# Kernel optimization log

Measured on AMD Instinct MI355X. Metric: run time of the kernel, lower is better.

The kernel has to match this reference:

```python
import jax, jax.numpy as jnp
import numpy as np

NUM_LEVELS = 16
LEVEL_DIM = 2
BASE_RES = 16
MAX_RES = 2048
HASHMAP_SIZE = 1 << 19
N_POINTS = 2000000

# Instant-NGP geometric progression of grid resolutions
_scale = np.exp2(np.log2(MAX_RES / BASE_RES) / (NUM_LEVELS - 1))
RESOLUTIONS = [int(np.ceil(BASE_RES * _scale ** l)) for l in range(NUM_LEVELS)]

# corner offsets of the unit cube, shape [8, 3]
_OFFS = np.stack(np.meshgrid([0, 1], [0, 1], [0, 1], indexing='ij'), -1).reshape(8, 3)
_PRIMES = np.array([1, 2654435761, 805459861], dtype=np.uint32)


def grid_encode(x, table):
    """x: [N,3] in [0,1]; table: [L, T, F] -> [N, L*F]."""
    offs = jnp.asarray(_OFFS, dtype=jnp.int32)          # [8,3]
    feats = []
    for l, res in enumerate(RESOLUTIONS):
        pos = x * (res - 1)                              # [N,3]
        pos_i = jnp.clip(jnp.floor(pos).astype(jnp.int32), 0, res - 2)
        frac = pos - pos_i.astype(pos.dtype)             # [N,3]
        corners = pos_i[:, None, :] + offs[None]         # [N,8,3]
        if res ** 3 <= HASHMAP_SIZE:
            # dense (collision-free) indexing for coarse levels
            idx = corners[..., 0] + res * (corners[..., 1] + res * corners[..., 2])
        else:
            # spatial hash: xor of coordinate * prime, mod table size
            c = corners.astype(jnp.uint32)
            h = (c[..., 0] * _PRIMES[0]) ^ (c[..., 1] * _PRIMES[1]) ^ (c[..., 2] * _PRIMES[2])
            idx = (h % jnp.uint32(HASHMAP_SIZE)).astype(jnp.int32)
        vals = table[l][idx]                             # [N,8,F] gather
        # multilinear interpolation weights per corner
        w = jnp.prod(jnp.where(offs[None].astype(bool), frac[:, None, :], 1.0 - frac[:, None, :]), axis=-1)  # [N,8]
        feats.append(jnp.einsum('nc,ncf->nf', w, vals))
    return jnp.concatenate(feats, axis=-1)               # [N, 32]


def setup_inputs() -> dict:
    key = jax.random.key(0)
    ks = jax.random.split(key, 6)
    x = jax.random.uniform(ks[0], (N_POINTS, 3), dtype=jnp.float32)
    table = jax.random.uniform(ks[1], (NUM_LEVELS, HASHMAP_SIZE, LEVEL_DIM),
                               dtype=jnp.float32, minval=-1e-4, maxval=1e-4)
    in_dim = NUM_LEVELS * LEVEL_DIM  # 32
    W1 = jax.random.normal(ks[2], (in_dim, 64), dtype=jnp.float32) / np.sqrt(in_dim)
    W2 = jax.random.normal(ks[3], (64, 64), dtype=jnp.float32) / 8.0
    W3 = jax.random.normal(ks[4], (64, 64), dtype=jnp.float32) / 8.0
    Wo = jax.random.normal(ks[5], (64, 1), dtype=jnp.float32) / 8.0
    z = lambda n: jnp.zeros((n,), dtype=jnp.float32)
    return {"x": x, "table": table, "W1": W1, "b1": z(64), "W2": W2, "b2": z(64),
            "W3": W3, "b3": z(64), "Wo": Wo, "bo": z(1)}


def reference(x, table, W1, b1, W2, b2, W3, b3, Wo, bo):
    h = grid_encode(x, table)                 # [N,32]
    h = jax.nn.relu(h @ W1 + b1)
    h = jax.nn.relu(h @ W2 + b2)
    h = jax.nn.relu(h @ W3 + b3)
    return h @ Wo + bo                        # [N,1]
```

## Files before the change

### kernel.cpp

```cpp
#include <hip/hip_runtime.h>
#include <hip/hip_fp16.h>
#include <cmath>
#include <cstdint>


#define HASH_SZ (1u << 19)
#define HMASK   (HASH_SZ - 1u)
#define PR2 2654435761u
#define PR3 805459861u

typedef float v2f __attribute__((ext_vector_type(2)));
typedef float v4f __attribute__((ext_vector_type(4)));
typedef v4f v4fu __attribute__((aligned(8)));
typedef v2f v2fu __attribute__((aligned(8)));
typedef short bf16x8 __attribute__((ext_vector_type(8)));
typedef float f32x4 __attribute__((ext_vector_type(4)));
typedef unsigned int u32;
typedef u32 u32x2 __attribute__((ext_vector_type(2)));
typedef u32 u32x4 __attribute__((ext_vector_type(4)));
typedef u32x4 u32x4u __attribute__((aligned(8)));

struct ResArr { int r[16]; };

__device__ __forceinline__ unsigned short bf16_rne(float f) {
    union { float f; unsigned u; } v; v.f = f;
    unsigned u = v.u;
    unsigned r = (u + 0x7fffu + ((u >> 16) & 1u)) >> 16;
    return (unsigned short)r;
}
__device__ __forceinline__ float bf16f(unsigned short h) {
    union { unsigned u; float f; } v; v.u = ((unsigned)h) << 16;
    return v.f;
}
__device__ __forceinline__ void split8(const float* x, bf16x8& hi, bf16x8& lo) {
    #pragma unroll
    for (int j = 0; j < 8; ++j) {
        union { float f; unsigned u; } v; v.f = x[j];
        const unsigned hu = v.u & 0xffff0000u;
        hi[j] = (short)(hu >> 16);
        union { unsigned u; float f; } hf; hf.u = hu;
        const float d = x[j] - hf.f;
        union { float f; unsigned u; } dv; dv.f = d;
        lo[j] = (short)((dv.u + 0x7fffu + ((dv.u >> 16) & 1u)) >> 16);
    }
}
__device__ __forceinline__ u32 rne16u(float f) {
    union { float f; u32 u; } v; v.f = f;
    return (v.u + 0x7fffu + ((v.u >> 16) & 1u)) >> 16;
}
__device__ __forceinline__ u32x2 pack_split2(float f0, float f1) {
    union { float f; u32 u; } a, b; a.f = f0; b.f = f1;
    const u32 h0 = a.u & 0xffff0000u, h1 = b.u & 0xffff0000u;
    union { u32 u; float f; } ha, hb; ha.u = h0; hb.u = h1;
    u32x2 r;
    r.x = (h0 >> 16) | h1;
    r.y = rne16u(f0 - ha.f) | (rne16u(f1 - hb.f) << 16);
    return r;
}

__device__ __forceinline__ u32 pkh(float f0, float f1) {
    const __half h0 = __float2half_rn(f0), h1 = __float2half_rn(f1);
    return (u32)__half_as_ushort(h0) | ((u32)__half_as_ushort(h1) << 16);
}
__device__ __forceinline__ v2f cvt2(u32 e) {
    __half2 h;
    *reinterpret_cast<u32*>(&h) = e;
    v2f r; r.x = __low2float(h); r.y = __high2float(h);
    return r;
}
__device__ __forceinline__ u32 sel4(u32x4 P, u32 k) {
    const u32 a = (k & 1u) ? P.y : P.x;
    const u32 b = (k & 1u) ? P.w : P.z;
    return (k & 2u) ? b : a;
}

__global__ __launch_bounds__(256, 8)
void cvt_table(const float* __restrict__ table, u32* __restrict__ tab16, int total)
{
    const int e0 = (blockIdx.x * 256 + threadIdx.x) * 4;
    if (e0 >= total) return;
    const v4f a = __builtin_nontemporal_load((const v4f*)(table + 2 * (size_t)e0));
    const v4f b = __builtin_nontemporal_load((const v4f*)(table + 2 * (size_t)e0 + 4));
    u32x4 o;
    o.x = pkh(a.x, a.y); o.y = pkh(a.z, a.w);
    o.z = pkh(b.x, b.y); o.w = pkh(b.z, b.w);
    *(u32x4*)(tab16 + e0) = o;
}

__device__ __forceinline__ void gather16_one(
    const u32* __restrict__ tab, int res, bool dense,
    float px, float py, float pz, float& A0, float& A1)
{
    const float rf = (float)(res - 1);
    const float fx = px * rf, fy = py * rf, fz = pz * rf;
    int ix = (int)floorf(fx), iy = (int)floorf(fy), iz = (int)floorf(fz);
    ix = min(max(ix, 0), res - 2);
    iy = min(max(iy, 0), res - 2);
    iz = min(max(iz, 0), res - 2);
    const float tx = fx - (float)ix, ty = fy - (float)iy, tz = fz - (float)iz;
    const float sx = 1.f - tx, sy = 1.f - ty, sz = 1.f - tz;
    float a0 = 0.f, a1 = 0.f;

    if (dense) {
        const int b0 = ix + res * (iy + res * iz);
        #pragma unroll
        for (int c = 0; c < 4; ++c) {
            const int dy = c >> 1, dz = c & 1;
            const u32 idx0 = (u32)(b0 + res * dy + res * res * dz);
            const u32x4u Pv = *(const u32x4u*)(tab + (idx0 & ~1u));
            const bool hi = (idx0 & 1u) != 0u;
            const u32 e0 = hi ? Pv.y : Pv.x;
            const u32 e1 = hi ? Pv.z : Pv.y;
            const float wyz = (dy ? ty : sy) * (dz ? tz : sz);
            const float w0 = sx * wyz, w1 = tx * wyz;
            const v2f f0 = cvt2(e0), f1 = cvt2(e1);
            a0 = fmaf(w0, f0.x, a0); a1 = fmaf(w0, f0.y, a1);
            a0 = fmaf(w1, f1.x, a0); a1 = fmaf(w1, f1.y, a1);
        }
    } else {
        u32 i1a[4], k0[4];
        u32x4 P[4];
        #pragma unroll
        for (int c = 0; c < 4; ++c) {
            const int dy = c >> 1, dz = c & 1;
            const u32 r = (u32)(iy + dy) * PR2 ^ (u32)(iz + dz) * PR3;
            const u32 i0 = ((u32)ix ^ r) & HMASK;
            i1a[c] = ((u32)(ix + 1) ^ r) & HMASK;
            k0[c] = i0 & 3u;
            P[c] = *(const u32x4*)(tab + (i0 & ~3u));
        }
        const bool extra = ((ix & 3) == 3);
        u32 O[4];
        if (extra) {
            #pragma unroll
            for (int c = 0; c < 4; ++c) O[c] = tab[i1a[c]];
        } else {
            #pragma unroll
            for (int c = 0; c < 4; ++c) O[c] = 0u;
        }
        #pragma unroll
        for (int c = 0; c < 4; ++c) {
            const int dy = c >> 1, dz = c & 1;
            const u32 e0 = sel4(P[c], k0[c]);
            const u32 e1w = sel4(P[c], i1a[c] & 3u);
            const u32 e1 = extra ? O[c] : e1w;
            const float wyz = (dy ? ty : sy) * (dz ? tz : sz);
            const float w0 = sx * wyz, w1 = tx * wyz;
            const v2f f0 = cvt2(e0), f1 = cvt2(e1);
            a0 = fmaf(w0, f0.x, a0); a1 = fmaf(w0, f0.y, a1);
            a0 = fmaf(w1, f1.x, a0); a1 = fmaf(w1, f1.y, a1);
        }
    }
    A0 = a0; A1 = a1;
}

template<int NLEV>
__global__ __launch_bounds__(256, 8)
void encode16_k(const float* __restrict__ x, const u32* __restrict__ tab16,
                u32x2* __restrict__ featT, int n, int lb, ResArr rv)
{
    const int nth2 = gridDim.x * 512;
    for (int q = (blockIdx.x * 256 + threadIdx.x) * 2; q < n; q += nth2) {
        float p0x, p0y, p0z, p1x, p1y, p1z;
        const bool two = (q + 1 < n);
        if (two) {
            const v4fu a = __builtin_nontemporal_load((const v4fu*)(x + 3 * q));
            const v2f  b = __builtin_nontemporal_load((const v2fu*)(x + 3 * q + 4));
            p0x = a.x; p0y = a.y; p0z = a.z; p1x = a.w; p1y = b.x; p1z = b.y;
        } else {
            p0x = x[3 * q]; p0y = x[3 * q + 1]; p0z = x[3 * q + 2];
            p1x = p0x; p1y = p0y; p1z = p0z;
        }
        #pragma unroll
        for (int il = 0; il < NLEV; ++il) {
            const int l = lb + il;
            const int res = rv.r[l];
            const bool dense = ((long long)res * res * res <= (long long)HASH_SZ);
            const u32* tbl = tab16 + (size_t)l * HASH_SZ;
            float a00, a01, a10, a11;
            gather16_one(tbl, res, dense, p0x, p0y, p0z, a00, a01);
            gather16_one(tbl, res, dense, p1x, p1y, p1z, a10, a11);
            if (two) {
                const u32x2 e0 = pack_split2(a00, a01);
                const u32x2 e1 = pack_split2(a10, a11);
                u32x4 st; st.x = e0.x; st.y = e0.y; st.z = e1.x; st.w = e1.y;
                __builtin_nontemporal_store(st, (u32x4*)&featT[(size_t)l * n + q]);
            } else {
                __builtin_nontemporal_store(pack_split2(a00, a01),
                                            &featT[(size_t)l * n + q]);
            }
        }
    }
}

__device__ __forceinline__ void gather_one(
    const v2f* __restrict__ tbl, int res, bool dense,
    float px, float py, float pz, float& A0, float& A1)
{
    const float rf = (float)(res - 1);
    const float fx = px * rf, fy = py * rf, fz = pz * rf;
    int ix = (int)floorf(fx), iy = (int)floorf(fy), iz = (int)floorf(fz);
    ix = min(max(ix, 0), res - 2);
    iy = min(max(iy, 0), res - 2);
    iz = min(max(iz, 0), res - 2);
    const float tx = fx - (float)ix, ty = fy - (float)iy, tz = fz - (float)iz;
    const float sx = 1.f - tx, sy = 1.f - ty, sz = 1.f - tz;
    float a0 = 0.f, a1 = 0.f;

    if (dense) {
        const int b0 = ix + res * (iy + res * iz);
        v4fu P[4];
        #pragma unroll
        for (int c = 0; c < 4; ++c) {
            const int dy = c >> 1, dz = c & 1;
            P[c] = *(const v4fu*)((const float*)tbl + 2 * (b0 + res * dy + res * res * dz));
        }
        #pragma unroll
        for (int c = 0; c < 4; ++c) {
            const int dy = c >> 1, dz = c & 1;
            const float wyz = (dy ? ty : sy) * (dz ? tz : sz);
            const float w0 = sx * wyz, w1 = tx * wyz;
            a0 = fmaf(w0, P[c].x, a0); a1 = fmaf(w0, P[c].y, a1);
            a0 = fmaf(w1, P[c].z, a0); a1 = fmaf(w1, P[c].w, a1);
        }
    } else {
        uint32_t i0[4], i1[4];
        v4f P[4];
        #pragma unroll
        for (int c = 0; c < 4; ++c) {
            const int dy = c >> 1, dz = c & 1;
            const uint32_t r = (uint32_t)(iy + dy) * PR2 ^ (uint32_t)(iz + dz) * PR3;
            i0[c] = ((uint32_t)ix ^ r) & HMASK;
            i1[c] = ((uint32_t)(ix + 1) ^ r) & HMASK;
            P[c] = *(const v4f*)((const float*)tbl + 2 * (i0[c] & ~1u));
        }
        const bool odd = (ix & 1);
        v2f O[4];
        if (odd) {
            #pragma unroll
            for (int c = 0; c < 4; ++c) O[c] = tbl[i1[c]];
        } else {
            #pragma unroll
            for (int c = 0; c < 4; ++c) { v2f z = {0.f, 0.f}; O[c] = z; }
        }
        #pragma unroll
        for (int c = 0; c < 4; ++c) {
            const int dy = c >> 1, dz = c & 1;
            const bool hi = (i0[c] & 1);
            v2f c0, e;
            c0.x = hi ? P[c].z : P[c].x;  c0.y = hi ? P[c].w : P[c].y;
            e.x  = hi ? P[c].x : P[c].z;  e.y  = hi ? P[c].y : P[c].w;
            const v2f c1 = odd ? O[c] : e;
            const float wyz = (dy ? ty : sy) * (dz ? tz : sz);
            const float w0 = sx * wyz, w1 = tx * wyz;
            a0 = fmaf(w0, c0.x, a0); a1 = fmaf(w0, c0.y, a1);
            a0 = fmaf(w1, c1.x, a0); a1 = fmaf(w1, c1.y, a1);
        }
    }
    A0 = a0; A1 = a1;
}

template<int NLEV>
__global__ __launch_bounds__(256, 8)
void encode_k(const float* __restrict__ x, const float* __restrict__ table,
              u32x2* __restrict__ featT, int n, int lb, ResArr rv)
{
    const int nth2 = gridDim.x * 512;
    for (int q = (blockIdx.x * 256 + threadIdx.x) * 2; q < n; q += nth2) {
        float p0x, p0y, p0z, p1x, p1y, p1z;
        const bool two = (q + 1 < n);
        if (two) {
            const v4fu a = __builtin_nontemporal_load((const v4fu*)(x + 3 * q));
            const v2f  b = __builtin_nontemporal_load((const v2fu*)(x + 3 * q + 4));
            p0x = a.x; p0y = a.y; p0z = a.z; p1x = a.w; p1y = b.x; p1z = b.y;
        } else {
            p0x = x[3 * q]; p0y = x[3 * q + 1]; p0z = x[3 * q + 2];
            p1x = p0x; p1y = p0y; p1z = p0z;
        }
        #pragma unroll
        for (int il = 0; il < NLEV; ++il) {
            const int l = lb + il;
            const int res = rv.r[l];
            const bool dense = ((long long)res * res * res <= (long long)HASH_SZ);
            const v2f* tbl = (const v2f*)table + (size_t)l * HASH_SZ;
            float a00, a01, a10, a11;
            gather_one(tbl, res, dense, p0x, p0y, p0z, a00, a01);
            gather_one(tbl, res, dense, p1x, p1y, p1z, a10, a11);
            if (two) {
                const u32x2 e0 = pack_split2(a00, a01);
                const u32x2 e1 = pack_split2(a10, a11);
                u32x4 st; st.x = e0.x; st.y = e0.y; st.z = e1.x; st.w = e1.y;
                __builtin_nontemporal_store(st, (u32x4*)&featT[(size_t)l * n + q]);
            } else {
                __builtin_nontemporal_store(pack_split2(a00, a01),
                                            &featT[(size_t)l * n + q]);
            }
        }
    }
}

__global__ void prep_weights(const float* __restrict__ W1,
                             const float* __restrict__ W2,
                             const float* __restrict__ W3,
                             unsigned short* __restrict__ wb)
{
    const int tid = threadIdx.x;
    const int nb = tid >> 6, lane = tid & 63;
    const int l15 = lane & 15, q = lane >> 4;
    #pragma unroll
    for (int j = 0; j < 8; ++j) {
        const float v = W1[(q * 8 + j) * 64 + nb * 16 + l15];
        const unsigned short h = bf16_rne(v);
        wb[(nb * 64 + lane) * 8 + j] = h;
        wb[2048 + (nb * 64 + lane) * 8 + j] = bf16_rne(v - bf16f(h));
    }
    #pragma unroll
    for (int kb = 0; kb < 2; ++kb) {
        #pragma unroll
        for (int j = 0; j < 8; ++j) {
            const int row = kb * 32 + q * 8 + j;
            const int idx = ((kb * 4 + nb) * 64 + lane) * 8 + j;
            float v = W2[row * 64 + nb * 16 + l15];
            unsigned short h = bf16_rne(v);
            wb[4096 + idx] = h;
            wb[8192 + idx] = bf16_rne(v - bf16f(h));
            v = W3[row * 64 + nb * 16 + l15];
            h = bf16_rne(v);
            wb[12288 + idx] = h;
            wb[16384 + idx] = bf16_rne(v - bf16f(h));
        }
    }
}

__global__ __launch_bounds__(256, 4)
void mlp_mfma(const u32x2* __restrict__ featT,
              const unsigned short* __restrict__ wb,
              const float* __restrict__ b1, const float* __restrict__ b2,
              const float* __restrict__ b3,
              const float* __restrict__ Wo, const float* __restrict__ bo,
              float* __restrict__ out, int n)
{
    const int wave = threadIdx.x >> 6;
    const int lane = threadIdx.x & 63;
    const int l15 = lane & 15, quad = lane >> 4;
    const int p0 = (blockIdx.x * 4 + wave) * 32;
    if (p0 >= n) return;

    bf16x8 bh[2], bl[2];
    #pragma unroll
    for (int t = 0; t < 2; ++t) {
        const int p = p0 + t * 16 + l15;
        const int pl = (p < n) ? p : (n - 1);
        u32x4 hw, lw;
        #pragma unroll
        for (int jj = 0; jj < 4; ++jj) {
            const u32x2 v = featT[(size_t)(quad * 4 + jj) * n + pl];
            hw[jj] = v.x; lw[jj] = v.y;
        }
        bh[t] = *(bf16x8*)&hw;
        bl[t] = *(bf16x8*)&lw;
    }

    f32x4 acc[2][4];
    #pragma unroll
    for (int nb = 0; nb < 4; ++nb) {
        const bf16x8 wh = *(const bf16x8*)(wb + (nb * 64 + lane) * 8);
        const bf16x8 wl = *(const bf16x8*)(wb + 2048 + (nb * 64 + lane) * 8);
        const f32x4 bv = *(const f32x4*)(b1 + nb * 16 + quad * 4);
        #pragma unroll
        for (int t = 0; t < 2; ++t) {
            f32x4 c = bv;
            c = __builtin_amdgcn_mfma_f32_16x16x32_bf16(wh, bl[t], c, 0, 0, 0);
            c = __builtin_amdgcn_mfma_f32_16x16x32_bf16(wl, bh[t], c, 0, 0, 0);
            c = __builtin_amdgcn_mfma_f32_16x16x32_bf16(wh, bh[t], c, 0, 0, 0);
            acc[t][nb] = c;
        }
    }

    #pragma unroll
    for (int layer = 0; layer < 2; ++layer) {
        bf16x8 nh[2][2], nl[2][2];
        #pragma unroll
        for (int t = 0; t < 2; ++t) {
            #pragma unroll
            for (int kb = 0; kb < 2; ++kb) {
                float v[8];
                #pragma unroll
                for (int rr = 0; rr < 4; ++rr) {
                    float xq = fmaxf(acc[t][2 * kb][rr],     0.f);
                    float yq = fmaxf(acc[t][2 * kb + 1][rr], 0.f);
                    asm("v_permlane32_swap_b32 %0, %1" : "+v"(xq), "+v"(yq));
                    asm("v_permlane16_swap_b32 %0, %1" : "+v"(xq), "+v"(yq));
                    v[rr]     = xq;
                    v[4 + rr] = yq;
                }
                split8(v, nh[t][kb], nl[t][kb]);
            }
        }
        const int base_h = layer ? 12288 : 4096;
        const int base_l = layer ? 16384 : 8192;
        const float* __restrict__ bias = layer ? b3 : b2;
        #pragma unroll
        for (int nb = 0; nb < 4; ++nb) {
            const f32x4 bv = *(const f32x4*)(bias + nb * 16 + quad * 4);
            f32x4 c[2];
            #pragma unroll
            for (int t = 0; t < 2; ++t) c[t] = bv;
            #pragma unroll
            for (int kb = 0; kb < 2; ++kb) {
                const int idx = ((kb * 4 + nb) * 64 + lane) * 8;
                const bf16x8 wh = *(const bf16x8*)(wb + base_h + idx);
                const bf16x8 wl = *(const bf16x8*)(wb + base_l + idx);
                #pragma unroll
                for (int t = 0; t < 2; ++t) {
                    c[t] = __builtin_amdgcn_mfma_f32_16x16x32_bf16(wh, nl[t][kb], c[t], 0, 0, 0);
                    c[t] = __builtin_amdgcn_mfma_f32_16x16x32_bf16(wl, nh[t][kb], c[t], 0, 0, 0);
                    c[t] = __builtin_amdgcn_mfma_f32_16x16x32_bf16(wh, nh[t][kb], c[t], 0, 0, 0);
                }
            }
            #pragma unroll
            for (int t = 0; t < 2; ++t) acc[t][nb] = c[t];
        }
    }

    float part[2];
    #pragma unroll
    for (int t = 0; t < 2; ++t) {
        float s = 0.f;
        #pragma unroll
        for (int nb = 0; nb < 4; ++nb) {
            const f32x4 wo4 = *(const f32x4*)(Wo + nb * 16 + quad * 4);
            #pragma unroll
            for (int r = 0; r < 4; ++r)
                s = fmaf(fmaxf(acc[t][nb][r], 0.f), wo4[r], s);
        }
        part[t] = s;
    }
    #pragma unroll
    for (int t = 0; t < 2; ++t) {
        part[t] += __shfl_xor(part[t], 16, 64);
        part[t] += __shfl_xor(part[t], 32, 64);
    }
    if (quad == 0) {
        const float b = bo[0];
        #pragma unroll
        for (int t = 0; t < 2; ++t) {
            const int po = p0 + t * 16 + l15;
            if (po < n) out[po] = part[t] + b;
        }
    }
}

__global__ __launch_bounds__(256, 3)
void mlp_forward(const u32x2* __restrict__ featT,
                 const float* __restrict__ W1, const float* __restrict__ b1,
                 const float* __restrict__ W2, const float* __restrict__ b2,
                 const float* __restrict__ W3, const float* __restrict__ b3,
                 const float* __restrict__ Wo, const float* __restrict__ bo,
                 float* __restrict__ out, int n)
{
    const int p = blockIdx.x * 256 + threadIdx.x;
    if (p >= n) return;
    const v2f z2 = {0.f, 0.f};
    v2f A[32], B[32];
    #pragma unroll
    for (int jq = 0; jq < 16; ++jq) {
        const v4f b = *(const v4f*)(b1 + 4 * jq);
        A[2 * jq] = b.xy; A[2 * jq + 1] = b.zw;
    }
    #pragma unroll
    for (int l = 0; l < 16; ++l) {
        const u32x2 e = __builtin_nontemporal_load(&featT[(size_t)l * n + p]);
        union { u32 u; float f; } h0, h1, l0, l1;
        h0.u = e.x << 16; h1.u = e.x & 0xffff0000u;
        l0.u = e.y << 16; l1.u = e.y & 0xffff0000u;
        v2f f; f.x = h0.f + l0.f; f.y = h1.f + l1.f;
        const v4f* w0 = (const v4f*)(W1 + (size_t)(2 * l) * 64);
        const v4f* w1 = (const v4f*)(W1 + (size_t)(2 * l + 1) * 64);
        const v2f hh0 = {f.x, f.x}, hh1 = {f.y, f.y};
        #pragma unroll
        for (int jq = 0; jq < 16; ++jq) {
            const v4f wa = w0[jq];
            A[2 * jq]     = __builtin_elementwise_fma(hh0, wa.xy, A[2 * jq]);
            A[2 * jq + 1] = __builtin_elementwise_fma(hh0, wa.zw, A[2 * jq + 1]);
        }
        #pragma unroll
        for (int jq = 0; jq < 16; ++jq) {
            const v4f wb2 = w1[jq];
            A[2 * jq]     = __builtin_elementwise_fma(hh1, wb2.xy, A[2 * jq]);
            A[2 * jq + 1] = __builtin_elementwise_fma(hh1, wb2.zw, A[2 * jq + 1]);
        }
    }
    #pragma unroll
    for (int j = 0; j < 32; ++j) A[j] = __builtin_elementwise_max(A[j], z2);
    #pragma unroll
    for (int jq = 0; jq < 16; ++jq) {
        const v4f b = *(const v4f*)(b2 + 4 * jq);
        B[2 * jq] = b.xy; B[2 * jq + 1] = b.zw;
    }
    #pragma unroll
    for (int k = 0; k < 64; ++k) {
        const float hv = A[k >> 1][k & 1];
        const v2f h = {hv, hv};
        const v4f* w = (const v4f*)(W2 + (size_t)k * 64);
        #pragma unroll
        for (int jq = 0; jq < 16; ++jq) {
            const v4f wa = w[jq];
            B[2 * jq]     = __builtin_elementwise_fma(h, wa.xy, B[2 * jq]);
            B[2 * jq + 1] = __builtin_elementwise_fma(h, wa.zw, B[2 * jq + 1]);
        }
    }
    #pragma unroll
    for (int j = 0; j < 32; ++j) B[j] = __builtin_elementwise_max(B[j], z2);
    #pragma unroll
    for (int jq = 0; jq < 16; ++jq) {
        const v4f b = *(const v4f*)(b3 + 4 * jq);
        A[2 * jq] = b.xy; A[2 * jq + 1] = b.zw;
    }
    #pragma unroll
    for (int k = 0; k < 64; ++k) {
        const float hv = B[k >> 1][k & 1];
        const v2f h = {hv, hv};
        const v4f* w = (const v4f*)(W3 + (size_t)k * 64);
        #pragma unroll
        for (int jq = 0; jq < 16; ++jq) {
            const v4f wa = w[jq];
            A[2 * jq]     = __builtin_elementwise_fma(h, wa.xy, A[2 * jq]);
            A[2 * jq + 1] = __builtin_elementwise_fma(h, wa.zw, A[2 * jq + 1]);
        }
    }
    v2f o2 = z2;
    #pragma unroll
    for (int jq = 0; jq < 16; ++jq) {
        const v4f wa = *(const v4f*)(Wo + 4 * jq);
        o2 = __builtin_elementwise_fma(__builtin_elementwise_max(A[2 * jq], z2),     wa.xy, o2);
        o2 = __builtin_elementwise_fma(__builtin_elementwise_max(A[2 * jq + 1], z2), wa.zw, o2);
    }
    out[p] = o2.x + o2.y + bo[0];
}

__global__ __launch_bounds__(256, 2)
void hashpinn_fused(const float* __restrict__ x,
                    const float* __restrict__ table,
                    const float* __restrict__ W1, const float* __restrict__ b1,
                    const float* __restrict__ W2, const float* __restrict__ b2,
                    const float* __restrict__ W3, const float* __restrict__ b3,
                    const float* __restrict__ Wo, const float* __restrict__ bo,
                    float* __restrict__ out, int n, ResArr rv)
{
    const int p = blockIdx.x * 256 + threadIdx.x;
    if (p >= n) return;
    const float px = x[3*p+0], py = x[3*p+1], pz = x[3*p+2];
    float feat[32];
    #pragma unroll
    for (int l = 0; l < 16; ++l) {
        const int res = rv.r[l];
        const float rf = (float)(res - 1);
        const float fx = px*rf, fy = py*rf, fz = pz*rf;
        int ix=(int)floorf(fx), iy=(int)floorf(fy), iz=(int)floorf(fz);
        ix=min(max(ix,0),res-2); iy=min(max(iy,0),res-2); iz=min(max(iz,0),res-2);
        const float tx=fx-(float)ix, ty=fy-(float)iy, tz=fz-(float)iz;
        const float sx=1.f-tx, sy=1.f-ty, sz=1.f-tz;
        const float2* tbl=(const float2*)table+(size_t)l*HASH_SZ;
        const bool dense=((long long)res*res*res<=(long long)HASH_SZ);
        float a0=0.f, a1=0.f;
        #pragma unroll
        for (int c=0;c<8;++c){
            const uint32_t cx=(uint32_t)(ix+((c>>2)&1));
            const uint32_t cy=(uint32_t)(iy+((c>>1)&1));
            const uint32_t cz=(uint32_t)(iz+(c&1));
            uint32_t idx = dense ? cx+(uint32_t)res*(cy+(uint32_t)res*cz)
                                 : ((cx*1u ^ cy*PR2 ^ cz*PR3)&HMASK);
            const float2 v=tbl[idx];
            const float w=(((c>>2)&1)?tx:sx)*(((c>>1)&1)?ty:sy)*((c&1)?tz:sz);
            a0=fmaf(w,v.x,a0); a1=fmaf(w,v.y,a1);
        }
        feat[2*l]=a0; feat[2*l+1]=a1;
    }
    float A[64], B[64];
    #pragma unroll
    for (int j=0;j<64;++j) A[j]=b1[j];
    #pragma unroll
    for (int k=0;k<32;++k){ const float h=feat[k];
        #pragma unroll
        for (int j=0;j<64;++j) A[j]=fmaf(h,W1[k*64+j],A[j]); }
    #pragma unroll 1
    for (int it=0;it<2;++it){
        const float* W = it?W3:W2; const float* bb = it?b3:b2;
        #pragma unroll
        for (int j=0;j<64;++j){ A[j]=fmaxf(A[j],0.f); B[j]=bb[j]; }
        #pragma unroll
        for (int k=0;k<64;++k){ const float h=A[k];
            #pragma unroll
            for (int j=0;j<64;++j) B[j]=fmaf(h,W[k*64+j],B[j]); }
        #pragma unroll
        for (int j=0;j<64;++j) A[j]=B[j];
    }
    float o=bo[0];
    #pragma unroll
    for (int j=0;j<64;++j) o=fmaf(fmaxf(A[j],0.f),Wo[j],o);
    out[p]=o;
}

static inline void launch_encode16(int nlev, const float* x, const u32* tab16,
                                   u32x2* featT, int n, int lb, const ResArr& rv,
                                   hipStream_t stream) {
    const dim3 g(4096), b(256);
    switch (nlev) {
        case 1: hipLaunchKernelGGL(encode16_k<1>, g, b, 0, stream, x, tab16, featT, n, lb, rv); break;
        case 2: hipLaunchKernelGGL(encode16_k<2>, g, b, 0, stream, x, tab16, featT, n, lb, rv); break;
        case 3: hipLaunchKernelGGL(encode16_k<3>, g, b, 0, stream, x, tab16, featT, n, lb, rv); break;
        case 4: hipLaunchKernelGGL(encode16_k<4>, g, b, 0, stream, x, tab16, featT, n, lb, rv); break;
        case 5: hipLaunchKernelGGL(encode16_k<5>, g, b, 0, stream, x, tab16, featT, n, lb, rv); break;
        case 6: hipLaunchKernelGGL(encode16_k<6>, g, b, 0, stream, x, tab16, featT, n, lb, rv); break;
        case 7: hipLaunchKernelGGL(encode16_k<7>, g, b, 0, stream, x, tab16, featT, n, lb, rv); break;
        default: hipLaunchKernelGGL(encode16_k<8>, g, b, 0, stream, x, tab16, featT, n, lb, rv); break;
    }
}

static inline void launch_encode(int nlev, const float* x, const float* table,
                                 u32x2* featT, int n, int lb, const ResArr& rv,
                                 hipStream_t stream) {
    const dim3 g(4096), b(256);
    switch (nlev) {
        case 1: hipLaunchKernelGGL(encode_k<1>, g, b, 0, stream, x, table, featT, n, lb, rv); break;
        case 2: hipLaunchKernelGGL(encode_k<2>, g, b, 0, stream, x, table, featT, n, lb, rv); break;
        case 3: hipLaunchKernelGGL(encode_k<3>, g, b, 0, stream, x, table, featT, n, lb, rv); break;
        case 4: hipLaunchKernelGGL(encode_k<4>, g, b, 0, stream, x, table, featT, n, lb, rv); break;
        case 5: hipLaunchKernelGGL(encode_k<5>, g, b, 0, stream, x, table, featT, n, lb, rv); break;
        case 6: hipLaunchKernelGGL(encode_k<6>, g, b, 0, stream, x, table, featT, n, lb, rv); break;
        case 7: hipLaunchKernelGGL(encode_k<7>, g, b, 0, stream, x, table, featT, n, lb, rv); break;
        default: hipLaunchKernelGGL(encode_k<8>, g, b, 0, stream, x, table, featT, n, lb, rv); break;
    }
}

extern "C" void kernel_launch(void* const* d_in, const int* in_sizes, int n_in,
                              void* d_out, int out_size, void* d_ws, size_t ws_size,
                              hipStream_t stream) {
    const float* x     = (const float*)d_in[0];
    const float* table = (const float*)d_in[1];
    const float* W1    = (const float*)d_in[2];
    const float* b1    = (const float*)d_in[3];
    const float* W2    = (const float*)d_in[4];
    const float* b2    = (const float*)d_in[5];
    const float* W3    = (const float*)d_in[6];
    const float* b3    = (const float*)d_in[7];
    const float* Wo    = (const float*)d_in[8];
    const float* bo    = (const float*)d_in[9];
    float* out = (float*)d_out;

    const int n = in_sizes[0] / 3;

    ResArr rv;
    const double scale = std::exp2(std::log2(2048.0 / 16.0) / 15.0);
    for (int l = 0; l < 16; ++l)
        rv.r[l] = (int)std::ceil(16.0 * std::pow(scale, (double)l));

    int dense_end = 0;
    while (dense_end < 16) {
        long long r = rv.r[dense_end];
        if (r * r * r <= (long long)HASH_SZ) ++dense_end; else break;
    }
    if (dense_end > 8) dense_end = 8;

    const size_t feat_bytes = (size_t)n * 16 * sizeof(u32x2);
    const size_t wb_bytes = 20480 * sizeof(unsigned short);
    const size_t tab16_bytes = (size_t)16 * HASH_SZ * sizeof(u32);
    const int total_entries = 16 * (int)HASH_SZ;

    if (ws_size >= feat_bytes + wb_bytes + tab16_bytes) {
        u32x2* featT = (u32x2*)d_ws;
        unsigned short* wb = (unsigned short*)((char*)d_ws + feat_bytes);
        u32* tab16 = (u32*)((char*)d_ws + feat_bytes + wb_bytes);

        hipLaunchKernelGGL(prep_weights, dim3(1), dim3(256), 0, stream, W1, W2, W3, wb);
        hipLaunchKernelGGL(cvt_table, dim3(8192), dim3(256), 0, stream,
                           table, tab16, total_entries);

        if (dense_end > 0)
            launch_encode16(dense_end, x, tab16, featT, n, 0, rv, stream);
        for (int l = dense_end; l < 16; ++l)
            launch_encode16(1, x, tab16, featT, n, l, rv, stream);

        const int nblocks = (n + 127) / 128;
        hipLaunchKernelGGL(mlp_mfma, dim3(nblocks), dim3(256), 0, stream,
                           featT, wb, b1, b2, b3, Wo, bo, out, n);
    } else if (ws_size >= feat_bytes + wb_bytes) {
        u32x2* featT = (u32x2*)d_ws;
        unsigned short* wb = (unsigned short*)((char*)d_ws + feat_bytes);

        hipLaunchKernelGGL(prep_weights, dim3(1), dim3(256), 0, stream, W1, W2, W3, wb);

        if (dense_end > 0)
            launch_encode(dense_end, x, table, featT, n, 0, rv, stream);
        for (int l = dense_end; l < 16; ++l)
            launch_encode(1, x, table, featT, n, l, rv, stream);

        const int nblocks = (n + 127) / 128;
        hipLaunchKernelGGL(mlp_mfma, dim3(nblocks), dim3(256), 0, stream,
                           featT, wb, b1, b2, b3, Wo, bo, out, n);
    } else if (ws_size >= feat_bytes) {
        u32x2* featT = (u32x2*)d_ws;
        if (dense_end > 0)
            launch_encode(dense_end, x, table, featT, n, 0, rv, stream);
        for (int l = dense_end; l < 16; ++l)
            launch_encode(1, x, table, featT, n, l, rv, stream);
        hipLaunchKernelGGL(mlp_forward, dim3((n + 255) / 256), dim3(256), 0, stream,
                           featT, W1, b1, W2, b2, W3, b3, Wo, bo, out, n);
    } else {
        hipLaunchKernelGGL(hashpinn_fused, dim3((n + 255) / 256), dim3(256), 0, stream,
                           x, table, W1, b1, W2, b2, W3, b3, Wo, bo, out, n, rv);
    }
}
```

Before: 1.077 ms.

## Process points in two halves to shrink feature buffer and keep it cache-resident

Splits the point set into two halves, encoding and running the MLP on each half in turn, so the intermediate feature buffer is half the size and uses a stride parameter. The aim is for the feature writes and reads to stay more in the large last-level cache and cut HBM traffic. The encode grid is also resized to match the point count instead of a fixed 4096 blocks. This doubles the number of kernel launches and adds a serialization point between halves.

```diff
diff --git a/kernel.cpp b/kernel.cpp
--- a/kernel.cpp
+++ b/kernel.cpp
@@ -157,7 +157,7 @@
 template<int NLEV>
 __global__ __launch_bounds__(256, 8)
 void encode16_k(const float* __restrict__ x, const u32* __restrict__ tab16,
-                u32x2* __restrict__ featT, int n, int lb, ResArr rv)
+                u32x2* __restrict__ featT, int n, int ns, int lb, ResArr rv)
 {
     const int nth2 = gridDim.x * 512;
     for (int q = (blockIdx.x * 256 + threadIdx.x) * 2; q < n; q += nth2) {
@@ -184,10 +184,10 @@
                 const u32x2 e0 = pack_split2(a00, a01);
                 const u32x2 e1 = pack_split2(a10, a11);
                 u32x4 st; st.x = e0.x; st.y = e0.y; st.z = e1.x; st.w = e1.y;
-                __builtin_nontemporal_store(st, (u32x4*)&featT[(size_t)l * n + q]);
+                __builtin_nontemporal_store(st, (u32x4*)&featT[(size_t)l * ns + q]);
             } else {
                 __builtin_nontemporal_store(pack_split2(a00, a01),
-                                            &featT[(size_t)l * n + q]);
+                                            &featT[(size_t)l * ns + q]);
             }
         }
     }
@@ -338,7 +338,7 @@
               const float* __restrict__ b1, const float* __restrict__ b2,
               const float* __restrict__ b3,
               const float* __restrict__ Wo, const float* __restrict__ bo,
-              float* __restrict__ out, int n)
+              float* __restrict__ out, int n, int ns)
 {
     const int wave = threadIdx.x >> 6;
     const int lane = threadIdx.x & 63;
@@ -354,7 +354,7 @@
         u32x4 hw, lw;
         #pragma unroll
         for (int jj = 0; jj < 4; ++jj) {
-            const u32x2 v = featT[(size_t)(quad * 4 + jj) * n + pl];
+            const u32x2 v = featT[(size_t)(quad * 4 + jj) * ns + pl];
             hw[jj] = v.x; lw[jj] = v.y;
         }
         bh[t] = *(bf16x8*)&hw;
@@ -603,18 +603,18 @@
 }
 
 static inline void launch_encode16(int nlev, const float* x, const u32* tab16,
-                                   u32x2* featT, int n, int lb, const ResArr& rv,
-                                   hipStream_t stream) {
-    const dim3 g(4096), b(256);
+                                   u32x2* featT, int n, int ns, int lb,
+                                   const ResArr& rv, hipStream_t stream) {
+    const dim3 g((n + 511) / 512), b(256);
     switch (nlev) {
-        case 1: hipLaunchKernelGGL(encode16_k<1>, g, b, 0, stream, x, tab16, featT, n, lb, rv); break;
-        case 2: hipLaunchKernelGGL(encode16_k<2>, g, b, 0, stream, x, tab16, featT, n, lb, rv); break;
-        case 3: hipLaunchKernelGGL(encode16_k<3>, g, b, 0, stream, x, tab16, featT, n, lb, rv); break;
-        case 4: hipLaunchKernelGGL(encode16_k<4>, g, b, 0, stream, x, tab16, featT, n, lb, rv); break;
-        case 5: hipLaunchKernelGGL(encode16_k<5>, g, b, 0, stream, x, tab16, featT, n, lb, rv); break;
-        case 6: hipLaunchKernelGGL(encode16_k<6>, g, b, 0, stream, x, tab16, featT, n, lb, rv); break;
-        case 7: hipLaunchKernelGGL(encode16_k<7>, g, b, 0, stream, x, tab16, featT, n, lb, rv); break;
-        default: hipLaunchKernelGGL(encode16_k<8>, g, b, 0, stream, x, tab16, featT, n, lb, rv); break;
+        case 1: hipLaunchKernelGGL(encode16_k<1>, g, b, 0, stream, x, tab16, featT, n, ns, lb, rv); break;
+        case 2: hipLaunchKernelGGL(encode16_k<2>, g, b, 0, stream, x, tab16, featT, n, ns, lb, rv); break;
+        case 3: hipLaunchKernelGGL(encode16_k<3>, g, b, 0, stream, x, tab16, featT, n, ns, lb, rv); break;
+        case 4: hipLaunchKernelGGL(encode16_k<4>, g, b, 0, stream, x, tab16, featT, n, ns, lb, rv); break;
+        case 5: hipLaunchKernelGGL(encode16_k<5>, g, b, 0, stream, x, tab16, featT, n, ns, lb, rv); break;
+        case 6: hipLaunchKernelGGL(encode16_k<6>, g, b, 0, stream, x, tab16, featT, n, ns, lb, rv); break;
+        case 7: hipLaunchKernelGGL(encode16_k<7>, g, b, 0, stream, x, tab16, featT, n, ns, lb, rv); break;
+        default: hipLaunchKernelGGL(encode16_k<8>, g, b, 0, stream, x, tab16, featT, n, ns, lb, rv); break;
     }
 }
 
@@ -663,28 +663,46 @@
     }
     if (dense_end > 8) dense_end = 8;
 
-    const size_t feat_bytes = (size_t)n * 16 * sizeof(u32x2);
     const size_t wb_bytes = 20480 * sizeof(unsigned short);
     const size_t tab16_bytes = (size_t)16 * HASH_SZ * sizeof(u32);
     const int total_entries = 16 * (int)HASH_SZ;
 
-    if (ws_size >= feat_bytes + wb_bytes + tab16_bytes) {
+    int h0 = ((n + 1) / 2 + 1) & ~1;
+    if (h0 > n) h0 = n;
+    const int h1 = n - h0;
+    const int ns0 = (h0 + 1) & ~1;
+    const int ns1 = (h1 + 1) & ~1;
+    const int nsmax = ns0 > ns1 ? ns0 : ns1;
+    const size_t feat_half_bytes = (size_t)nsmax * 16 * sizeof(u32x2);
+
+    const size_t feat_bytes = (size_t)n * 16 * sizeof(u32x2);
+
+    if (ws_size >= feat_half_bytes + wb_bytes + tab16_bytes) {
         u32x2* featT = (u32x2*)d_ws;
-        unsigned short* wb = (unsigned short*)((char*)d_ws + feat_bytes);
-        u32* tab16 = (u32*)((char*)d_ws + feat_bytes + wb_bytes);
+        unsigned short* wb = (unsigned short*)((char*)d_ws + feat_half_bytes);
+        u32* tab16 = (u32*)((char*)d_ws + feat_half_bytes + wb_bytes);
 
         hipLaunchKernelGGL(prep_weights, dim3(1), dim3(256), 0, stream, W1, W2, W3, wb);
         hipLaunchKernelGGL(cvt_table, dim3(8192), dim3(256), 0, stream,
                            table, tab16, total_entries);
 
-        if (dense_end > 0)
-            launch_encode16(dense_end, x, tab16, featT, n, 0, rv, stream);
-        for (int l = dense_end; l < 16; ++l)
-            launch_encode16(1, x, tab16, featT, n, l, rv, stream);
-
-        const int nblocks = (n + 127) / 128;
-        hipLaunchKernelGGL(mlp_mfma, dim3(nblocks), dim3(256), 0, stream,
-                           featT, wb, b1, b2, b3, Wo, bo, out, n);
+        #pragma unroll
+        for (int half = 0; half < 2; ++half) {
+            const int off = half ? h0 : 0;
+            const int nh  = half ? h1 : h0;
+            const int ns  = half ? ns1 : ns0;
+            if (nh <= 0) continue;
+            const float* xh = x + (size_t)3 * off;
+
+            if (dense_end > 0)
+                launch_encode16(dense_end, xh, tab16, featT, nh, ns, 0, rv, stream);
+            for (int l = dense_end; l < 16; ++l)
+                launch_encode16(1, xh, tab16, featT, nh, ns, l, rv, stream);
+
+            const int nblocks = (nh + 127) / 128;
+            hipLaunchKernelGGL(mlp_mfma, dim3(nblocks), dim3(256), 0, stream,
+                               featT, wb, b1, b2, b3, Wo, bo, out + off, nh, ns);
+        }
     } else if (ws_size >= feat_bytes + wb_bytes) {
         u32x2* featT = (u32x2*)d_ws;
         unsigned short* wb = (unsigned short*)((char*)d_ws + feat_bytes);
@@ -698,7 +716,7 @@
 
         const int nblocks = (n + 127) / 128;
         hipLaunchKernelGGL(mlp_mfma, dim3(nblocks), dim3(256), 0, stream,
-                           featT, wb, b1, b2, b3, Wo, bo, out, n);
+                           featT, wb, b1, b2, b3, Wo, bo, out, n, n);
     } else if (ws_size >= feat_bytes) {
         u32x2* featT = (u32x2*)d_ws;
         if (dense_end > 0)
```

New measurement: 981.8 us. 8.8% less time.

## Split points into quarters and overlap encoding with the previous quarter's MLP

Applied to the files above, without the earlier changes.

Points are processed in four chunks. Each chunk's hash-grid encoding runs in the same launch as the MLP for the previous chunk, with the work types interleaved or placed side by side across blocks. Features go into two double-buffered slabs, which shrinks the feature workspace so it can stay resident in cache. The encoder now launches one block range per level instead of one kernel per hashed level, so a single launch covers all 16 levels. This cuts launch count and lets the gather-bound encode overlap the MFMA MLP. The cost is more complex indexing and occupancy limited by launch bounds of 4.

```diff
diff --git a/kernel.cpp b/kernel.cpp
--- a/kernel.cpp
+++ b/kernel.cpp
@@ -154,41 +154,226 @@
     A0 = a0; A1 = a1;
 }
 
-template<int NLEV>
-__global__ __launch_bounds__(256, 8)
-void encode16_k(const float* __restrict__ x, const u32* __restrict__ tab16,
-                u32x2* __restrict__ featT, int n, int lb, ResArr rv)
-{
-    const int nth2 = gridDim.x * 512;
-    for (int q = (blockIdx.x * 256 + threadIdx.x) * 2; q < n; q += nth2) {
+__global__ void prep_weights(const float* __restrict__ W1,
+                             const float* __restrict__ W2,
+                             const float* __restrict__ W3,
+                             unsigned short* __restrict__ wb)
+{
+    const int tid = threadIdx.x;
+    const int nb = tid >> 6, lane = tid & 63;
+    const int l15 = lane & 15, q = lane >> 4;
+    #pragma unroll
+    for (int j = 0; j < 8; ++j) {
+        const float v = W1[(q * 8 + j) * 64 + nb * 16 + l15];
+        const unsigned short h = bf16_rne(v);
+        wb[(nb * 64 + lane) * 8 + j] = h;
+        wb[2048 + (nb * 64 + lane) * 8 + j] = bf16_rne(v - bf16f(h));
+    }
+    #pragma unroll
+    for (int kb = 0; kb < 2; ++kb) {
+        #pragma unroll
+        for (int j = 0; j < 8; ++j) {
+            const int row = kb * 32 + q * 8 + j;
+            const int idx = ((kb * 4 + nb) * 64 + lane) * 8 + j;
+            float v = W2[row * 64 + nb * 16 + l15];
+            unsigned short h = bf16_rne(v);
+            wb[4096 + idx] = h;
+            wb[8192 + idx] = bf16_rne(v - bf16f(h));
+            v = W3[row * 64 + nb * 16 + l15];
+            h = bf16_rne(v);
+            wb[12288 + idx] = h;
+            wb[16384 + idx] = bf16_rne(v - bf16f(h));
+        }
+    }
+}
+
+__device__ __forceinline__ void mlp_block(
+    const u32x2* __restrict__ featT,
+    const unsigned short* __restrict__ wb,
+    const float* __restrict__ b1, const float* __restrict__ b2,
+    const float* __restrict__ b3,
+    const float* __restrict__ Wo, const float* __restrict__ bo,
+    float* __restrict__ out, int n, int ns, int mb)
+{
+    const int wave = threadIdx.x >> 6;
+    const int lane = threadIdx.x & 63;
+    const int l15 = lane & 15, quad = lane >> 4;
+    const int p0 = (mb * 4 + wave) * 32;
+    if (p0 >= n) return;
+
+    bf16x8 bh[2], bl[2];
+    #pragma unroll
+    for (int t = 0; t < 2; ++t) {
+        const int p = p0 + t * 16 + l15;
+        const int pl = (p < n) ? p : (n - 1);
+        u32x4 hw, lw;
+        #pragma unroll
+        for (int jj = 0; jj < 4; ++jj) {
+            const u32x2 v = featT[(size_t)(quad * 4 + jj) * ns + pl];
+            hw[jj] = v.x; lw[jj] = v.y;
+        }
+        bh[t] = *(bf16x8*)&hw;
+        bl[t] = *(bf16x8*)&lw;
+    }
+
+    f32x4 acc[2][4];
+    #pragma unroll
+    for (int nb = 0; nb < 4; ++nb) {
+        const bf16x8 wh = *(const bf16x8*)(wb + (nb * 64 + lane) * 8);
+        const bf16x8 wl = *(const bf16x8*)(wb + 2048 + (nb * 64 + lane) * 8);
+        const f32x4 bv = *(const f32x4*)(b1 + nb * 16 + quad * 4);
+        #pragma unroll
+        for (int t = 0; t < 2; ++t) {
+            f32x4 c = bv;
+            c = __builtin_amdgcn_mfma_f32_16x16x32_bf16(wh, bl[t], c, 0, 0, 0);
+            c = __builtin_amdgcn_mfma_f32_16x16x32_bf16(wl, bh[t], c, 0, 0, 0);
+            c = __builtin_amdgcn_mfma_f32_16x16x32_bf16(wh, bh[t], c, 0, 0, 0);
+            acc[t][nb] = c;
+        }
+    }
+
+    #pragma unroll
+    for (int layer = 0; layer < 2; ++layer) {
+        bf16x8 nh[2][2], nl[2][2];
+        #pragma unroll
+        for (int t = 0; t < 2; ++t) {
+            #pragma unroll
+            for (int kb = 0; kb < 2; ++kb) {
+                float v[8];
+                #pragma unroll
+                for (int rr = 0; rr < 4; ++rr) {
+                    float xq = fmaxf(acc[t][2 * kb][rr],     0.f);
+                    float yq = fmaxf(acc[t][2 * kb + 1][rr], 0.f);
+                    asm("v_permlane32_swap_b32 %0, %1" : "+v"(xq), "+v"(yq));
+                    asm("v_permlane16_swap_b32 %0, %1" : "+v"(xq), "+v"(yq));
+                    v[rr]     = xq;
+                    v[4 + rr] = yq;
+                }
+                split8(v, nh[t][kb], nl[t][kb]);
+            }
+        }
+        const int base_h = layer ? 12288 : 4096;
+        const int base_l = layer ? 16384 : 8192;
+        const float* __restrict__ bias = layer ? b3 : b2;
+        #pragma unroll
+        for (int nb = 0; nb < 4; ++nb) {
+            const f32x4 bv = *(const f32x4*)(bias + nb * 16 + quad * 4);
+            f32x4 c[2];
+            #pragma unroll
+            for (int t = 0; t < 2; ++t) c[t] = bv;
+            #pragma unroll
+            for (int kb = 0; kb < 2; ++kb) {
+                const int idx = ((kb * 4 + nb) * 64 + lane) * 8;
+                const bf16x8 wh = *(const bf16x8*)(wb + base_h + idx);
+                const bf16x8 wl = *(const bf16x8*)(wb + base_l + idx);
+                #pragma unroll
+                for (int t = 0; t < 2; ++t) {
+                    c[t] = __builtin_amdgcn_mfma_f32_16x16x32_bf16(wh, nl[t][kb], c[t], 0, 0, 0);
+                    c[t] = __builtin_amdgcn_mfma_f32_16x16x32_bf16(wl, nh[t][kb], c[t], 0, 0, 0);
+                    c[t] = __builtin_amdgcn_mfma_f32_16x16x32_bf16(wh, nh[t][kb], c[t], 0, 0, 0);
+                }
+            }
+            #pragma unroll
+            for (int t = 0; t < 2; ++t) acc[t][nb] = c[t];
+        }
+    }
+
+    float part[2];
+    #pragma unroll
+    for (int t = 0; t < 2; ++t) {
+        float s = 0.f;
+        #pragma unroll
+        for (int nb = 0; nb < 4; ++nb) {
+            const f32x4 wo4 = *(const f32x4*)(Wo + nb * 16 + quad * 4);
+            #pragma unroll
+            for (int r = 0; r < 4; ++r)
+                s = fmaf(fmaxf(acc[t][nb][r], 0.f), wo4[r], s);
+        }
+        part[t] = s;
+    }
+    #pragma unroll
+    for (int t = 0; t < 2; ++t) {
+        part[t] += __shfl_xor(part[t], 16, 64);
+        part[t] += __shfl_xor(part[t], 32, 64);
+    }
+    if (quad == 0) {
+        const float b = bo[0];
+        #pragma unroll
+        for (int t = 0; t < 2; ++t) {
+            const int po = p0 + t * 16 + l15;
+            if (po < n) out[po] = part[t] + b;
+        }
+    }
+}
+
+__global__ __launch_bounds__(256, 4)
+void mlp_mfma(const u32x2* __restrict__ featT,
+              const unsigned short* __restrict__ wb,
+              const float* __restrict__ b1, const float* __restrict__ b2,
+              const float* __restrict__ b3,
+              const float* __restrict__ Wo, const float* __restrict__ bo,
+              float* __restrict__ out, int n, int ns)
+{
+    mlp_block(featT, wb, b1, b2, b3, Wo, bo, out, n, ns, blockIdx.x);
+}
+
+__global__ __launch_bounds__(256, 4)
+void fused_q(const float* __restrict__ xe, const u32* __restrict__ tab16,
+             u32x2* __restrict__ fe, int ne, int nse,
+             const u32x2* __restrict__ fm,
+             const unsigned short* __restrict__ wb,
+             const float* __restrict__ b1, const float* __restrict__ b2,
+             const float* __restrict__ b3,
+             const float* __restrict__ Wo, const float* __restrict__ bo,
+             float* __restrict__ outm, int nm, int nsm,
+             ResArr rv, int de, int bpl, int M, int ilv)
+{
+    const int b = blockIdx.x;
+    int eb;
+    if (ilv) {
+        const int q4 = b >> 2, r4 = b & 3;
+        if (r4 == 3 && q4 < M) {
+            mlp_block(fm, wb, b1, b2, b3, Wo, bo, outm, nm, nsm, q4);
+            return;
+        }
+        eb = b - ((r4 == 3) ? M : min(q4, M));
+    } else {
+        if (b < M) {
+            mlp_block(fm, wb, b1, b2, b3, Wo, bo, outm, nm, nsm, b);
+            return;
+        }
+        eb = b - M;
+    }
+    const int lvl = eb / bpl;
+    if (lvl >= 16) return;
+    const int lblk = eb - lvl * bpl;
+    const int res = rv.r[lvl];
+    const bool dense = (lvl < de);
+    const u32* tbl = tab16 + (size_t)lvl * HASH_SZ;
+
+    const int nth2 = bpl * 512;
+    for (int q = (lblk * 256 + (int)threadIdx.x) * 2; q < ne; q += nth2) {
         float p0x, p0y, p0z, p1x, p1y, p1z;
-        const bool two = (q + 1 < n);
+        const bool two = (q + 1 < ne);
         if (two) {
-            const v4fu a = __builtin_nontemporal_load((const v4fu*)(x + 3 * q));
-            const v2f  b = __builtin_nontemporal_load((const v2fu*)(x + 3 * q + 4));
-            p0x = a.x; p0y = a.y; p0z = a.z; p1x = a.w; p1y = b.x; p1z = b.y;
+            const v4fu a = __builtin_nontemporal_load((const v4fu*)(xe + 3 * q));
+            const v2f  bb = __builtin_nontemporal_load((const v2fu*)(xe + 3 * q + 4));
+            p0x = a.x; p0y = a.y; p0z = a.z; p1x = a.w; p1y = bb.x; p1z = bb.y;
         } else {
-            p0x = x[3 * q]; p0y = x[3 * q + 1]; p0z = x[3 * q + 2];
+            p0x = xe[3 * q]; p0y = xe[3 * q + 1]; p0z = xe[3 * q + 2];
             p1x = p0x; p1y = p0y; p1z = p0z;
         }
-        #pragma unroll
-        for (int il = 0; il < NLEV; ++il) {
-            const int l = lb + il;
-            const int res = rv.r[l];
-            const bool dense = ((long long)res * res * res <= (long long)HASH_SZ);
-            const u32* tbl = tab16 + (size_t)l * HASH_SZ;
-            float a00, a01, a10, a11;
-            gather16_one(tbl, res, dense, p0x, p0y, p0z, a00, a01);
-            gather16_one(tbl, res, dense, p1x, p1y, p1z, a10, a11);
-            if (two) {
-                const u32x2 e0 = pack_split2(a00, a01);
-                const u32x2 e1 = pack_split2(a10, a11);
-                u32x4 st; st.x = e0.x; st.y = e0.y; st.z = e1.x; st.w = e1.y;
-                __builtin_nontemporal_store(st, (u32x4*)&featT[(size_t)l * n + q]);
-            } else {
-                __builtin_nontemporal_store(pack_split2(a00, a01),
-                                            &featT[(size_t)l * n + q]);
-            }
+        float a00, a01, a10, a11;
+        gather16_one(tbl, res, dense, p0x, p0y, p0z, a00, a01);
+        gather16_one(tbl, res, dense, p1x, p1y, p1z, a10, a11);
+        if (two) {
+            const u32x2 e0 = pack_split2(a00, a01);
+            const u32x2 e1 = pack_split2(a10, a11);
+            u32x4 st; st.x = e0.x; st.y = e0.y; st.z = e1.x; st.w = e1.y;
+            __builtin_nontemporal_store(st, (u32x4*)&fe[(size_t)lvl * nse + q]);
+        } else {
+            __builtin_nontemporal_store(pack_split2(a00, a01),
+                                        &fe[(size_t)lvl * nse + q]);
         }
     }
 }
@@ -299,158 +484,6 @@
     }
 }
 
-__global__ void prep_weights(const float* __restrict__ W1,
-                             const float* __restrict__ W2,
-                             const float* __restrict__ W3,
-                             unsigned short* __restrict__ wb)
-{
-    const int tid = threadIdx.x;
-    const int nb = tid >> 6, lane = tid & 63;
-    const int l15 = lane & 15, q = lane >> 4;
-    #pragma unroll
-    for (int j = 0; j < 8; ++j) {
-        const float v = W1[(q * 8 + j) * 64 + nb * 16 + l15];
-        const unsigned short h = bf16_rne(v);
-        wb[(nb * 64 + lane) * 8 + j] = h;
-        wb[2048 + (nb * 64 + lane) * 8 + j] = bf16_rne(v - bf16f(h));
-    }
-    #pragma unroll
-    for (int kb = 0; kb < 2; ++kb) {
-        #pragma unroll
-        for (int j = 0; j < 8; ++j) {
-            const int row = kb * 32 + q * 8 + j;
-            const int idx = ((kb * 4 + nb) * 64 + lane) * 8 + j;
-            float v = W2[row * 64 + nb * 16 + l15];
-            unsigned short h = bf16_rne(v);
-            wb[4096 + idx] = h;
-            wb[8192 + idx] = bf16_rne(v - bf16f(h));
-            v = W3[row * 64 + nb * 16 + l15];
-            h = bf16_rne(v);
-            wb[12288 + idx] = h;
-            wb[16384 + idx] = bf16_rne(v - bf16f(h));
-        }
-    }
-}
-
-__global__ __launch_bounds__(256, 4)
-void mlp_mfma(const u32x2* __restrict__ featT,
-              const unsigned short* __restrict__ wb,
-              const float* __restrict__ b1, const float* __restrict__ b2,
-              const float* __restrict__ b3,
-              const float* __restrict__ Wo, const float* __restrict__ bo,
-              float* __restrict__ out, int n)
-{
-    const int wave = threadIdx.x >> 6;
-    const int lane = threadIdx.x & 63;
-    const int l15 = lane & 15, quad = lane >> 4;
-    const int p0 = (blockIdx.x * 4 + wave) * 32;
-    if (p0 >= n) return;
-
-    bf16x8 bh[2], bl[2];
-    #pragma unroll
-    for (int t = 0; t < 2; ++t) {
-        const int p = p0 + t * 16 + l15;
-        const int pl = (p < n) ? p : (n - 1);
-        u32x4 hw, lw;
-        #pragma unroll
-        for (int jj = 0; jj < 4; ++jj) {
-            const u32x2 v = featT[(size_t)(quad * 4 + jj) * n + pl];
-            hw[jj] = v.x; lw[jj] = v.y;
-        }
-        bh[t] = *(bf16x8*)&hw;
-        bl[t] = *(bf16x8*)&lw;
-    }
-
-    f32x4 acc[2][4];
-    #pragma unroll
-    for (int nb = 0; nb < 4; ++nb) {
-        const bf16x8 wh = *(const bf16x8*)(wb + (nb * 64 + lane) * 8);
-        const bf16x8 wl = *(const bf16x8*)(wb + 2048 + (nb * 64 + lane) * 8);
-        const f32x4 bv = *(const f32x4*)(b1 + nb * 16 + quad * 4);
-        #pragma unroll
-        for (int t = 0; t < 2; ++t) {
-            f32x4 c = bv;
-            c = __builtin_amdgcn_mfma_f32_16x16x32_bf16(wh, bl[t], c, 0, 0, 0);
-            c = __builtin_amdgcn_mfma_f32_16x16x32_bf16(wl, bh[t], c, 0, 0, 0);
-            c = __builtin_amdgcn_mfma_f32_16x16x32_bf16(wh, bh[t], c, 0, 0, 0);
-            acc[t][nb] = c;
-        }
-    }
-
-    #pragma unroll
-    for (int layer = 0; layer < 2; ++layer) {
-        bf16x8 nh[2][2], nl[2][2];
-        #pragma unroll
-        for (int t = 0; t < 2; ++t) {
-            #pragma unroll
-            for (int kb = 0; kb < 2; ++kb) {
-                float v[8];
-                #pragma unroll
-                for (int rr = 0; rr < 4; ++rr) {
-                    float xq = fmaxf(acc[t][2 * kb][rr],     0.f);
-                    float yq = fmaxf(acc[t][2 * kb + 1][rr], 0.f);
-                    asm("v_permlane32_swap_b32 %0, %1" : "+v"(xq), "+v"(yq));
-                    asm("v_permlane16_swap_b32 %0, %1" : "+v"(xq), "+v"(yq));
-                    v[rr]     = xq;
-                    v[4 + rr] = yq;
-                }
-                split8(v, nh[t][kb], nl[t][kb]);
-            }
-        }
-        const int base_h = layer ? 12288 : 4096;
-        const int base_l = layer ? 16384 : 8192;
-        const float* __restrict__ bias = layer ? b3 : b2;
-        #pragma unroll
-        for (int nb = 0; nb < 4; ++nb) {
-            const f32x4 bv = *(const f32x4*)(bias + nb * 16 + quad * 4);
-            f32x4 c[2];
-            #pragma unroll
-            for (int t = 0; t < 2; ++t) c[t] = bv;
-            #pragma unroll
-            for (int kb = 0; kb < 2; ++kb) {
-                const int idx = ((kb * 4 + nb) * 64 + lane) * 8;
-                const bf16x8 wh = *(const bf16x8*)(wb + base_h + idx);
-                const bf16x8 wl = *(const bf16x8*)(wb + base_l + idx);
-                #pragma unroll
-                for (int t = 0; t < 2; ++t) {
-                    c[t] = __builtin_amdgcn_mfma_f32_16x16x32_bf16(wh, nl[t][kb], c[t], 0, 0, 0);
-                    c[t] = __builtin_amdgcn_mfma_f32_16x16x32_bf16(wl, nh[t][kb], c[t], 0, 0, 0);
-                    c[t] = __builtin_amdgcn_mfma_f32_16x16x32_bf16(wh, nh[t][kb], c[t], 0, 0, 0);
-                }
-            }
-            #pragma unroll
-            for (int t = 0; t < 2; ++t) acc[t][nb] = c[t];
-        }
-    }
-
-    float part[2];
-    #pragma unroll
-    for (int t = 0; t < 2; ++t) {
-        float s = 0.f;
-        #pragma unroll
-        for (int nb = 0; nb < 4; ++nb) {
-            const f32x4 wo4 = *(const f32x4*)(Wo + nb * 16 + quad * 4);
-            #pragma unroll
-            for (int r = 0; r < 4; ++r)
-                s = fmaf(fmaxf(acc[t][nb][r], 0.f), wo4[r], s);
-        }
-        part[t] = s;
-    }
-    #pragma unroll
-    for (int t = 0; t < 2; ++t) {
-        part[t] += __shfl_xor(part[t], 16, 64);
-        part[t] += __shfl_xor(part[t], 32, 64);
-    }
-    if (quad == 0) {
-        const float b = bo[0];
-        #pragma unroll
-        for (int t = 0; t < 2; ++t) {
-            const int po = p0 + t * 16 + l15;
-            if (po < n) out[po] = part[t] + b;
-        }
-    }
-}
-
 __global__ __launch_bounds__(256, 3)
 void mlp_forward(const u32x2* __restrict__ featT,
                  const float* __restrict__ W1, const float* __restrict__ b1,
@@ -600,22 +633,6 @@
     #pragma unroll
     for (int j=0;j<64;++j) o=fmaf(fmaxf(A[j],0.f),Wo[j],o);
     out[p]=o;
-}
-
-static inline void launch_encode16(int nlev, const float* x, const u32* tab16,
-                                   u32x2* featT, int n, int lb, const ResArr& rv,
-                                   hipStream_t stream) {
-    const dim3 g(4096), b(256);
-    switch (nlev) {
-        case 1: hipLaunchKernelGGL(encode16_k<1>, g, b, 0, stream, x, tab16, featT, n, lb, rv); break;
-        case 2: hipLaunchKernelGGL(encode16_k<2>, g, b, 0, stream, x, tab16, featT, n, lb, rv); break;
-        case 3: hipLaunchKernelGGL(encode16_k<3>, g, b, 0, stream, x, tab16, featT, n, lb, rv); break;
-        case 4: hipLaunchKernelGGL(encode16_k<4>, g, b, 0, stream, x, tab16, featT, n, lb, rv); break;
-        case 5: hipLaunchKernelGGL(encode16_k<5>, g, b, 0, stream, x, tab16, featT, n, lb, rv); break;
-        case 6: hipLaunchKernelGGL(encode16_k<6>, g, b, 0, stream, x, tab16, featT, n, lb, rv); break;
-        case 7: hipLaunchKernelGGL(encode16_k<7>, g, b, 0, stream, x, tab16, featT, n, lb, rv); break;
-        default: hipLaunchKernelGGL(encode16_k<8>, g, b, 0, stream, x, tab16, featT, n, lb, rv); break;
-    }
 }
 
 static inline void launch_encode(int nlev, const float* x, const float* table,
@@ -663,28 +680,71 @@
     }
     if (dense_end > 8) dense_end = 8;
 
-    const size_t feat_bytes = (size_t)n * 16 * sizeof(u32x2);
     const size_t wb_bytes = 20480 * sizeof(unsigned short);
     const size_t tab16_bytes = (size_t)16 * HASH_SZ * sizeof(u32);
     const int total_entries = 16 * (int)HASH_SZ;
 
-    if (ws_size >= feat_bytes + wb_bytes + tab16_bytes) {
-        u32x2* featT = (u32x2*)d_ws;
-        unsigned short* wb = (unsigned short*)((char*)d_ws + feat_bytes);
-        u32* tab16 = (u32*)((char*)d_ws + feat_bytes + wb_bytes);
+    const int Q = 4;
+    int qoff[Q + 1];
+    {
+        int base = ((n + Q - 1) / Q + 1) & ~1;
+        for (int i = 0; i <= Q; ++i) {
+            long long o = (long long)base * i;
+            qoff[i] = (int)(o < n ? o : n);
+        }
+        qoff[Q] = n;
+    }
+    int nsmax = 2;
+    for (int i = 0; i < Q; ++i) {
+        const int nq = qoff[i + 1] - qoff[i];
+        const int ns = (nq + 1) & ~1;
+        if (ns > nsmax) nsmax = ns;
+    }
+    const size_t slab_bytes = (size_t)nsmax * 16 * sizeof(u32x2);
+    const size_t feat_bytes = (size_t)n * 16 * sizeof(u32x2);
+
+    if (ws_size >= 2 * slab_bytes + wb_bytes + tab16_bytes) {
+        u32x2* fA = (u32x2*)d_ws;
+        u32x2* fB = (u32x2*)((char*)d_ws + slab_bytes);
+        unsigned short* wb = (unsigned short*)((char*)d_ws + 2 * slab_bytes);
+        u32* tab16 = (u32*)((char*)d_ws + 2 * slab_bytes + wb_bytes);
 
         hipLaunchKernelGGL(prep_weights, dim3(1), dim3(256), 0, stream, W1, W2, W3, wb);
         hipLaunchKernelGGL(cvt_table, dim3(8192), dim3(256), 0, stream,
                            table, tab16, total_entries);
 
-        if (dense_end > 0)
-            launch_encode16(dense_end, x, tab16, featT, n, 0, rv, stream);
-        for (int l = dense_end; l < 16; ++l)
-            launch_encode16(1, x, tab16, featT, n, l, rv, stream);
-
-        const int nblocks = (n + 127) / 128;
-        hipLaunchKernelGGL(mlp_mfma, dim3(nblocks), dim3(256), 0, stream,
-                           featT, wb, b1, b2, b3, Wo, bo, out, n);
+        int prev_n = 0, prev_ns = 0, prev_off = 0;
+        for (int i = 0; i < Q; ++i) {
+            const int nq = qoff[i + 1] - qoff[i];
+            const int ns = (nq + 1) & ~1;
+            u32x2* cur = (i & 1) ? fB : fA;
+            u32x2* prv = (i & 1) ? fA : fB;
+            const int M = prev_n > 0 ? (prev_n + 127) / 128 : 0;
+            if (nq <= 0) {
+                if (M > 0)
+                    hipLaunchKernelGGL(mlp_mfma, dim3(M), dim3(256), 0, stream,
+                                       prv, wb, b1, b2, b3, Wo, bo,
+                                       out + prev_off, prev_n, prev_ns);
+                prev_n = 0;
+                continue;
+            }
+            const int bpl = (nq + 511) / 512;
+            const int T = 16 * bpl + M;
+            const int ilv = (M > 0 && 4 * M <= T) ? 1 : 0;
+            hipLaunchKernelGGL(fused_q, dim3(T), dim3(256), 0, stream,
+                               x + (size_t)3 * qoff[i], tab16, cur, nq, ns,
+                               prv, wb, b1, b2, b3, Wo, bo,
+                               out + prev_off, prev_n, prev_ns,
+                               rv, dense_end, bpl, M, ilv);
+            prev_n = nq; prev_ns = ns; prev_off = qoff[i];
+        }
+        if (prev_n > 0) {
+            u32x2* last = ((Q - 1) & 1) ? fB : fA;
+            const int M = (prev_n + 127) / 128;
+            hipLaunchKernelGGL(mlp_mfma, dim3(M), dim3(256), 0, stream,
+                               last, wb, b1, b2, b3, Wo, bo,
+                               out + prev_off, prev_n, prev_ns);
+        }
     } else if (ws_size >= feat_bytes + wb_bytes) {
         u32x2* featT = (u32x2*)d_ws;
         unsigned short* wb = (unsigned short*)((char*)d_ws + feat_bytes);
@@ -698,7 +758,7 @@
 
         const int nblocks = (n + 127) / 128;
         hipLaunchKernelGGL(mlp_mfma, dim3(nblocks), dim3(256), 0, stream,
-                           featT, wb, b1, b2, b3, Wo, bo, out, n);
+                           featT, wb, b1, b2, b3, Wo, bo, out, n, n);
     } else if (ws_size >= feat_bytes) {
         u32x2* featT = (u32x2*)d_ws;
         if (dense_end > 0)
```

Measured after the change: 966.6 us. 10.2% less time.
